# Kernel tuning notes

Measured on AMD Instinct MI355X. Metric: run time of the kernel, lower is better.

Reference implementation:

```python
import jax, jax.numpy as jnp
import numpy as np
from jax import lax

DN = ('NCHW', 'OIHW', 'NCHW')
NUM_CODES = 8192


def _conv(x, w, b):
    # Conv2d(k=4, s=2, p=1)
    y = lax.conv_general_dilated(x, w, (2, 2), ((1, 1), (1, 1)), dimension_numbers=DN)
    return y + b[None, :, None, None]


def _convT(x, w, b):
    # ConvTranspose2d(k=4, s=2, p=1) as lhs-dilated conv; kernel already in equivalent OIHW layout
    y = lax.conv_general_dilated(x, w, (1, 1), ((2, 2), (2, 2)), lhs_dilation=(2, 2), dimension_numbers=DN)
    return y + b[None, :, None, None]


def _aff(x, s, b):
    # eval-mode BatchNorm folded to per-channel affine
    return x * s[None, :, None, None] + b[None, :, None, None]


def _forward(x, ew1, eb1, bn1s, bn1b, ew2, eb2, bn2s, bn2b, ew3, eb3, bn3s, bn3b, ew4, eb4, embed, cluster_size, dw1, db1, dbn1s, dbn1b, dw2, db2, dbn2s, dbn2b, dw3, db3, dbn3s, dbn3b, dw4, db4):
    sg = lax.stop_gradient
    embed = sg(embed)          # codebook is a torch buffer -> no grad
    cluster_size = sg(cluster_size)
    relu = jax.nn.relu
    # ---- Encoder: 4 stride-2 convs ----
    h = relu(_aff(_conv(x, ew1, eb1), bn1s, bn1b))
    h = relu(_aff(_conv(h, ew2, eb2), bn2s, bn2b))
    h = relu(_aff(_conv(h, ew3, eb3), bn3s, bn3b))
    z = _conv(h, ew4, eb4)                       # [B, D, G, G]
    zt = jnp.transpose(z, (0, 2, 3, 1))          # [B, G, G, D]
    D = zt.shape[-1]
    flat = zt.reshape(-1, D)                     # [N, D]
    N = flat.shape[0]
    # ---- VQ: pairwise squared distance + argmin codebook lookup ----
    dist = (flat * flat).sum(1, keepdims=True) - 2.0 * (flat @ embed.T) + (embed * embed).sum(1)[None, :]
    soft = jax.nn.softmax(-dist, axis=-1)        # temperature = 1.0
    codes = jnp.argmin(dist, axis=1)             # [N]
    zq = embed[codes]                            # [N, D]
    commitment_loss = jnp.mean((flat - sg(zq)) ** 2)
    codebook_loss = jnp.mean((zq - sg(flat)) ** 2)
    avg_soft = soft.mean(0)
    usage_entropy = -(avg_soft * jnp.log(avg_soft + 1e-10)).sum()
    diversity_loss = -usage_entropy / float(np.log(NUM_CODES))
    zq_st = flat + sg(zq - flat)                 # straight-through estimator
    zq_grid = jnp.transpose(zq_st.reshape(zt.shape), (0, 3, 1, 2))  # [B, D, G, G]
    # ---- Decoder: 4 stride-2 transposed convs ----
    h = relu(_aff(_convT(zq_grid, dw1, db1), dbn1s, dbn1b))
    h = relu(_aff(_convT(h, dw2, db2), dbn2s, dbn2b))
    h = relu(_aff(_convT(h, dw3, db3), dbn3s, dbn3b))
    recon = jax.nn.sigmoid(_convT(h, dw4, db4))
    recon_loss = jnp.mean((recon - x) ** 2)
    # ---- usage stats (no-grad in torch) ----
    hard_avg = jnp.zeros(NUM_CODES, flat.dtype).at[codes].add(1.0) / N
    perplexity = jnp.exp(-(hard_avg * jnp.log(hard_avg + 1e-10)).sum())
    active_codes = (cluster_size > 1).sum()
    codes_grid = codes.reshape(zt.shape[:-1])
    return (recon, recon_loss, codes_grid, zq_grid, commitment_loss, codebook_loss, diversity_loss, usage_entropy, perplexity, active_codes)


def setup_inputs() -> dict:
    keys = iter(jax.random.split(jax.random.key(0), 64))
    def randn(shape, s=1.0):
        return jax.random.normal(next(keys), shape, jnp.float32) * s
    def randu(shape):
        return jax.random.uniform(next(keys), shape, dtype=jnp.float32)
    B, H = 32, 256
    return {
        'x': randu((B, 1, H, H)),
        'ew1': randn((64, 1, 4, 4), 0.25), 'eb1': randn((64,), 0.1),
        'bn1s': randu((64,)), 'bn1b': randn((64,), 0.1),
        'ew2': randn((64, 64, 4, 4), 0.03), 'eb2': randn((64,), 0.1),
        'bn2s': randu((64,)), 'bn2b': randn((64,), 0.1),
        'ew3': randn((128, 64, 4, 4), 0.03), 'eb3': randn((128,), 0.1),
        'bn3s': randu((128,)), 'bn3b': randn((128,), 0.1),
        'ew4': randn((64, 128, 4, 4), 0.02), 'eb4': randn((64,), 0.1),
        'embed': randn((8192, 64), 0.5),
        'cluster_size': jnp.ones((8192,), jnp.float32),
        'dw1': randn((128, 64, 4, 4), 0.03), 'db1': randn((128,), 0.1),
        'dbn1s': randu((128,)), 'dbn1b': randn((128,), 0.1),
        'dw2': randn((64, 128, 4, 4), 0.02), 'db2': randn((64,), 0.1),
        'dbn2s': randu((64,)), 'dbn2b': randn((64,), 0.1),
        'dw3': randn((64, 64, 4, 4), 0.03), 'db3': randn((64,), 0.1),
        'dbn3s': randu((64,)), 'dbn3b': randn((64,), 0.1),
        'dw4': randn((1, 64, 4, 4), 0.03), 'db4': randn((1,), 0.1),
    }


def reference(x, ew1, eb1, bn1s, bn1b, ew2, eb2, bn2s, bn2b, ew3, eb3, bn3s, bn3b, ew4, eb4, embed, cluster_size, dw1, db1, dbn1s, dbn1b, dw2, db2, dbn2s, dbn2b, dw3, db3, dbn3s, dbn3b, dw4, db4):
    return _forward(x, ew1, eb1, bn1s, bn1b, ew2, eb2, bn2s, bn2b, ew3, eb3, bn3s, bn3b, ew4, eb4, embed, cluster_size, dw1, db1, dbn1s, dbn1b, dw2, db2, dbn2s, dbn2b, dw3, db3, dbn3s, dbn3b, dw4, db4)
```

## Files before the change

kernel.cpp:

```cpp
#include <hip/hip_runtime.h>
#include <cstdint>
#include <cstddef>


#define DEVI __device__ __forceinline__

typedef short  short8 __attribute__((ext_vector_type(8)));
typedef __bf16 bf16x8 __attribute__((ext_vector_type(8)));
typedef float  f32x16 __attribute__((ext_vector_type(16)));

DEVI f32x16 MFMA(bf16x8 a, bf16x8 b, f32x16 c){
  return __builtin_amdgcn_mfma_f32_32x32x16_bf16(a, b, c, 0, 0, 0);
}

DEVI ushort f2bf(float f){
  unsigned u = __float_as_uint(f);
  unsigned r = (u + 0x7FFFu + ((u >> 16) & 1u)) >> 16;
  return (ushort)r;
}
DEVI float bf2f(ushort h){ return __uint_as_float(((unsigned)h) << 16); }

union U8 { short8 s; bf16x8 b; };
DEVI bf16x8 ldg8u(const ushort* p){
  U8 u; u.s = *(const short8*)p; return u.b;
}

DEVI float wred64(float v){
  #pragma unroll
  for (int off=32; off>0; off>>=1) v += __shfl_down(v, off, 64);
  return v;
}

#define O_RECON     0
#define O_RLOSS     2097152
#define O_CODES     2097153
#define O_ZQ        2105345
#define O_COMMIT    2629633
#define O_CB        2629634
#define O_DIV       2629635
#define O_UE        2629636
#define O_PERP      2629637
#define O_ACT       2629638

#define WS_R1       0ull
#define A3H_OFF     0ull
#define A3M_OFF     8912896ull
#define A3L_OFF     17825792ull
#define PP_OFF      33554432ull
#define MT_OFF      37748736ull
#define PARTA_OFF   41943040ull
#define A2H_OFF     134217728ull
#define A2M_OFF     151519232ull
#define A2L_OFF     168820736ull
#define EH_OFF      134217728ull
#define EM_OFF      135266304ull
#define EL_OFF      136314880ull
#define FH_OFF      137363456ull
#define FM_OFF      138412032ull
#define FL_OFF      139460608ull
#define D2H_OFF     134217728ull
#define D2L_OFF     151519232ull
#define D1H_OFF     168820736ull
#define D1L_OFF     177733632ull
#define WS_FLAT     186646528ull
#define WS_ZQP      188743680ull
#define WS_WT       191102976ull
#define WT_E2       (WS_WT)
#define WT_E3       (WT_E2 + 393216ull)
#define WT_E4       (WT_E3 + 786432ull)
#define WT_D1       (WT_E4 + 786432ull)
#define WT_D2       (WT_D1 + 524288ull)
#define WT_D3       (WT_D2 + 524288ull)
#define WS_W4       (WT_D3 + 262144ull)
#define WS_STATS    (WS_W4 + 4096ull)
#define ST_RMP      (WS_STATS)
#define ST_CNT      (ST_RMP + 65536ull)
#define ST_AVGS     (ST_CNT + 32768ull)
#define ST_ROWZI    (ST_AVGS + 32768ull)
#define ST_CODESQ   (ST_ROWZI + 32768ull)
#define ST_LOSS     (ST_CODESQ + 32768ull)
#define ST_ROWM     (ST_LOSS + 32768ull)

__global__ __launch_bounds__(256) void k_init(unsigned int* __restrict__ cnt,
                                              unsigned long long* __restrict__ rmp,
                                              float* __restrict__ loss)
{
  int i = blockIdx.x*256 + threadIdx.x;
  if (i < 8192){ cnt[i]=0u; rmp[i]=0xFFFFFFFFFFFFFFFFull; }
  if (i < 8) loss[i]=0.f;
}

__global__ __launch_bounds__(256) void k_wsplit(
    const float* __restrict__ src, ushort* __restrict__ dh,
    ushort* __restrict__ dm, ushort* __restrict__ dl,
    int OC, int CIN, int isT, int three)
{
  int i = blockIdx.x*256 + threadIdx.x;
  if (i >= 16*OC*CIN) return;
  int cin = i % CIN; int t = i / CIN; int oc = t % OC; int tap = t / OC;
  int st;
  if (isT){
    int pq = tap>>2, ab = tap&3;
    int p = pq>>1, q = pq&1, a = ab>>1, b = ab&1;
    st = (p + 2*a)*4 + (q + 2*b);
  } else st = tap;
  float v = src[((size_t)oc*CIN + cin)*16 + st];
  ushort h = f2bf(v); float r = v - bf2f(h);
  if (three){
    ushort m = f2bf(r); float r2 = r - bf2f(m);
    dm[i] = m; dl[i] = f2bf(r2);
  } else {
    dl[i] = f2bf(r);
  }
  dh[i] = h;
}

__global__ __launch_bounds__(256) void k_w4prep(const float* __restrict__ dw4,
                                                float* __restrict__ w4)
{
  int i = blockIdx.x*256 + threadIdx.x;
  if (i >= 1024) return;
  int c = i & 63; int t16 = i >> 6;
  int pq = t16 >> 2, ab = t16 & 3;
  int p = pq>>1, q = pq&1, a = ab>>1, b = ab&1;
  w4[i] = dw4[(size_t)c*16 + (p+2*a)*4 + (q+2*b)];
}

__global__ __launch_bounds__(256) void k_esplit(
    const float* __restrict__ src, ushort* __restrict__ dh,
    ushort* __restrict__ dm, ushort* __restrict__ dl)
{
  int i = blockIdx.x*256 + threadIdx.x;
  float v = src[i];
  ushort h = f2bf(v); float r1 = v - bf2f(h);
  ushort m = f2bf(r1); float r2 = r1 - bf2f(m);
  dh[i] = h; dm[i] = m; dl[i] = f2bf(r2);
}

__global__ __launch_bounds__(256) void k_zpad3(unsigned* __restrict__ b0,
                                               unsigned* __restrict__ b1,
                                               unsigned* __restrict__ b2,
                                               int rows, int Wp, int cwords)
{
  int i = blockIdx.x*256 + threadIdx.x;
  int total = rows*2*cwords;
  if (i >= total) return;
  int pos = i / cwords, cw = i % cwords;
  int row = pos >> 1, side = pos & 1;
  size_t w = ((size_t)row*Wp + (side ? (Wp-1) : 0))*cwords + cw;
  b0[w] = 0u;
  if (b1) b1[w] = 0u;
  if (b2) b2[w] = 0u;
}

__global__ __launch_bounds__(256) void enc_conv1(
    const float* __restrict__ x, const float* __restrict__ w,
    const float* __restrict__ cb_, const float* __restrict__ bns,
    const float* __restrict__ bnb, float* __restrict__ out)
{
  __shared__ __align__(16) float sIn[34][36];
  __shared__ __align__(16) float sW[64][16];
  int b = blockIdx.x;
  int t = b & 63, n = b >> 6;
  int ty = t >> 3, tx = t & 7;
  int oy0 = ty*16, ox0 = tx*16;
  int iy0 = 2*oy0 - 1, ix0 = 2*ox0 - 1;
  int tid = threadIdx.x;
  int spg = tid & 31, og = tid >> 5;
  int sy = spg >> 1, x0 = (spg & 1)*8;

  if (tid < 64){
    const float* wp = w + tid*16;
    *(float4*)&sW[tid][0]  = *(const float4*)(wp);
    *(float4*)&sW[tid][4]  = *(const float4*)(wp+4);
    *(float4*)&sW[tid][8]  = *(const float4*)(wp+8);
    *(float4*)&sW[tid][12] = *(const float4*)(wp+12);
  }
  for (int e = tid; e < 34*34; e += 256){
    int rr = e/34, cc = e%34;
    int iy = iy0+rr, ix = ix0+cc;
    float v = 0.f;
    if ((unsigned)iy < 256u && (unsigned)ix < 256u)
      v = x[(size_t)n*65536 + iy*256 + ix];
    sIn[rr][cc] = v;
  }
  __syncthreads();

  float acc[8][8];
  #pragma unroll
  for (int j=0;j<8;j++)
    #pragma unroll
    for (int xi=0;xi<8;xi++) acc[j][xi]=0.f;

  #pragma unroll
  for (int ky=0; ky<4; ky++){
    int riy = 2*sy + ky;
    float seg[20];
    #pragma unroll
    for (int i=0;i<5;i++){
      float4 v = *(const float4*)&sIn[riy][2*x0 + 4*i];
      seg[4*i+0]=v.x; seg[4*i+1]=v.y; seg[4*i+2]=v.z; seg[4*i+3]=v.w;
    }
    #pragma unroll
    for (int j=0;j<8;j++){
      float4 w4v = *(const float4*)&sW[og*8+j][ky*4];
      #pragma unroll
      for (int xi=0; xi<8; xi++){
        acc[j][xi] = fmaf(seg[2*xi+0], w4v.x,
                     fmaf(seg[2*xi+1], w4v.y,
                     fmaf(seg[2*xi+2], w4v.z,
                     fmaf(seg[2*xi+3], w4v.w, acc[j][xi]))));
      }
    }
  }

  float sc[8], sh[8];
  #pragma unroll
  for (int j=0;j<8;j++){
    int oc = og*8+j;
    sc[j] = bns[oc];
    sh[j] = fmaf(cb_[oc], sc[j], bnb[oc]);
  }
  int oy = oy0 + sy;
  #pragma unroll
  for (int xi=0; xi<8; xi++){
    int oxg = ox0 + x0 + xi;
    float* op = out + (((size_t)n*128 + oy)*128 + oxg)*64 + og*8;
    float4 q0, q1;
    q0.x = fmaxf(fmaf(acc[0][xi], sc[0], sh[0]), 0.f);
    q0.y = fmaxf(fmaf(acc[1][xi], sc[1], sh[1]), 0.f);
    q0.z = fmaxf(fmaf(acc[2][xi], sc[2], sh[2]), 0.f);
    q0.w = fmaxf(fmaf(acc[3][xi], sc[3], sh[3]), 0.f);
    q1.x = fmaxf(fmaf(acc[4][xi], sc[4], sh[4]), 0.f);
    q1.y = fmaxf(fmaf(acc[5][xi], sc[5], sh[5]), 0.f);
    q1.z = fmaxf(fmaf(acc[6][xi], sc[6], sh[6]), 0.f);
    q1.w = fmaxf(fmaf(acc[7][xi], sc[7], sh[7]), 0.f);
    *(float4*)op     = q0;
    *(float4*)(op+4) = q1;
  }
}

template<int CIN, int OC, int OUTW, int OUTH, int INW, int INH, bool XPAD,
         int INMODE, int OUTMODE>
__global__ __launch_bounds__(256) void enc_conv(
    const float* __restrict__ in,
    const ushort* __restrict__ aH, const ushort* __restrict__ aM,
    const ushort* __restrict__ aL,
    const ushort* __restrict__ wtH, const ushort* __restrict__ wtM,
    const ushort* __restrict__ wtL,
    const float* __restrict__ cb_, const float* __restrict__ bns,
    const float* __restrict__ bnb,
    float* __restrict__ outF,
    ushort* __restrict__ oH, ushort* __restrict__ oM, ushort* __restrict__ oL,
    int nOcg)
{
  constexpr int INWP  = (INMODE==1) ? (INW+2) : (XPAD ? (INW+2) : INW);
  constexpr int WP    = INW + 2;
  constexpr int NROWS = 64 / OUTW;
  constexpr int AELEM = NROWS * WP * CIN;
  constexpr int BCIN  = (CIN > 64) ? 64 : CIN;
  constexpr int BELEM = 64 * BCIN;
  constexpr int SCRSZ = (3*BELEM*2 > 64*68*4) ? 3*BELEM*2 : 64*68*4;

  __shared__ __align__(16) ushort sAh[AELEM], sAm[AELEM], sAl[AELEM];
  __shared__ __align__(16) char sScr[SCRSZ];
  ushort* sBh = (ushort*)sScr;
  ushort* sBm = sBh + BELEM;
  ushort* sBl = sBm + BELEM;
  float*  sC  = (float*)sScr;

  int b = blockIdx.x;
  int ocg = b % nOcg; b /= nOcg;
  int yb  = b % (OUTH/NROWS); b /= (OUTH/NROWS);
  int n = b;
  int oy0 = yb * NROWS, oc0 = ocg * 64;

  int tid = threadIdx.x;
  int l = tid & 63, wave = tid >> 6;
  int wm = wave >> 1, wn = wave & 1;
  int r = l & 31, kp = l >> 5;
  int idx = wm*32 + r;
  int oy_off = idx / OUTW, ox = idx % OUTW;

  f32x16 acc;
  #pragma unroll
  for (int i=0;i<16;i++) acc[i] = 0.f;

  const size_t nbase = (size_t)n * INH * INWP * CIN;

  for (int ky = 0; ky < 4; ky++){
    __syncthreads();
    for (int c = tid; c < AELEM/8; c += 256){
      int j  = c / (WP*CIN/8);
      int rm = c % (WP*CIN/8);
      int lx = rm / (CIN/8);
      int c8 = (rm % (CIN/8)) * 8;
      int iy = 2*(oy0 + j) - 1 + ky;
      bool ok = (unsigned)iy < (unsigned)INH;
      unsigned off = (unsigned)(((j*WP + lx)*CIN + c8)*2) ^ ((((unsigned)lx>>1)&7u)<<4);
      if constexpr (INMODE == 0){
        int gx = XPAD ? lx : (lx - 1);
        if (!XPAD) ok = ok && ((unsigned)gx < (unsigned)INW);
        float4 v0 = {0,0,0,0}, v1 = {0,0,0,0};
        if (ok){
          const float* s = in + nbase + ((size_t)iy*INWP + gx)*CIN + c8;
          v0 = *(const float4*)s; v1 = *(const float4*)(s+4);
        }
        float vv[8] = {v0.x,v0.y,v0.z,v0.w,v1.x,v1.y,v1.z,v1.w};
        short8 hh, mm, ll;
        #pragma unroll
        for (int e=0;e<8;e++){
          ushort h = f2bf(vv[e]); float r1 = vv[e] - bf2f(h);
          ushort m = f2bf(r1);    float r2 = r1 - bf2f(m);
          hh[e] = (short)h; mm[e] = (short)m; ll[e] = (short)f2bf(r2);
        }
        *(short8*)((char*)sAh + off) = hh;
        *(short8*)((char*)sAm + off) = mm;
        *(short8*)((char*)sAl + off) = ll;
      } else {
        short8 vh = {0,0,0,0,0,0,0,0}, vm = vh, vl = vh;
        if (ok){
          size_t s = nbase + ((size_t)iy*INWP + lx)*CIN + c8;
          vh = *(const short8*)(aH + s);
          vm = *(const short8*)(aM + s);
          vl = *(const short8*)(aL + s);
        }
        *(short8*)((char*)sAh + off) = vh;
        *(short8*)((char*)sAm + off) = vm;
        *(short8*)((char*)sAl + off) = vl;
      }
    }
    for (int kx = 0; kx < 4; kx++){
      int tap = ky*4 + kx;
      for (int ch = 0; ch < CIN; ch += BCIN){
        __syncthreads();
        for (int c = tid; c < BELEM/8; c += 256){
          int oc = c / (BCIN/8);
          int c8 = (c % (BCIN/8)) * 8;
          size_t s = ((size_t)tap*OC + oc0 + oc)*CIN + ch + c8;
          unsigned off = (unsigned)((oc*BCIN + c8)*2) ^ (((unsigned)oc&7u)<<4);
          *(short8*)((char*)sBh + off) = *(const short8*)(wtH + s);
          *(short8*)((char*)sBm + off) = *(const short8*)(wtM + s);
          *(short8*)((char*)sBl + off) = *(const short8*)(wtL + s);
        }
        __syncthreads();
        int lx = 2*ox + kx;
        unsigned asw  = ((((unsigned)lx>>1)&7u)<<4);
        unsigned alin = (unsigned)(((oy_off*WP + lx)*CIN)*2);
        int ocl = wn*32 + r;
        unsigned bsw  = (((unsigned)ocl&7u)<<4);
        unsigned blin = (unsigned)((ocl*BCIN)*2);
        #pragma unroll
        for (int ct = 0; ct < BCIN/16; ct++){
          unsigned kbA = (unsigned)((ch + ct*16 + kp*8)*2);
          unsigned kbB = (unsigned)((ct*16 + kp*8)*2);
          unsigned ao = (alin + kbA) ^ asw;
          unsigned bo = (blin + kbB) ^ bsw;
          bf16x8 ah = *(const bf16x8*)((char*)sAh + ao);
          bf16x8 am = *(const bf16x8*)((char*)sAm + ao);
          bf16x8 al = *(const bf16x8*)((char*)sAl + ao);
          bf16x8 bh = *(const bf16x8*)((char*)sBh + bo);
          bf16x8 bm = *(const bf16x8*)((char*)sBm + bo);
          bf16x8 bl = *(const bf16x8*)((char*)sBl + bo);
          acc = MFMA(ah, bh, acc);
          acc = MFMA(ah, bm, acc);
          acc = MFMA(am, bh, acc);
          acc = MFMA(ah, bl, acc);
          acc = MFMA(am, bm, acc);
          acc = MFMA(al, bh, acc);
        }
      }
    }
  }
  __syncthreads();
  #pragma unroll
  for (int q = 0; q < 16; q++){
    int rowt = (q&3) + 8*(q>>2) + 4*kp;
    sC[(wm*32 + rowt)*68 + wn*32 + r] = acc[q];
  }
  __syncthreads();
  {
    int m = tid >> 2, qq = tid & 3;
    int oc = oc0 + qq*16;
    int oyg = oy0 + m / OUTW;
    int oxg = m % OUTW;
    if constexpr (OUTMODE == 1){
      size_t row = (size_t)n*256 + oyg*16 + oxg;
      float* op = outF + row*64 + qq*16;
      size_t pb = row*64 + qq*16;
      short8 hv[2], mv[2], lv[2];
      #pragma unroll
      for (int i=0;i<16;i++){
        float v = sC[m*68 + qq*16 + i] + cb_[oc+i];
        op[i] = v;
        ushort h = f2bf(v); float r1 = v - bf2f(h);
        ushort mm = f2bf(r1); float r2 = r1 - bf2f(mm);
        hv[i>>3][i&7]=(short)h; mv[i>>3][i&7]=(short)mm; lv[i>>3][i&7]=(short)f2bf(r2);
      }
      *(short8*)(oH + pb) = hv[0]; *(short8*)(oH + pb + 8) = hv[1];
      *(short8*)(oM + pb) = mv[0]; *(short8*)(oM + pb + 8) = mv[1];
      *(short8*)(oL + pb) = lv[0]; *(short8*)(oL + pb + 8) = lv[1];
    } else {
      size_t pbase = (((size_t)n*OUTH + oyg)*(OUTW+2) + oxg + 1)*OC + oc;
      short8 hv[2], mv[2], lv[2];
      #pragma unroll
      for (int i=0;i<16;i++){
        float s1 = bns[oc+i];
        float s2 = fmaf(cb_[oc+i], s1, bnb[oc+i]);
        float v = fmaxf(fmaf(sC[m*68 + qq*16 + i], s1, s2), 0.f);
        ushort h = f2bf(v); float r1 = v - bf2f(h);
        ushort mm = f2bf(r1); float r2 = r1 - bf2f(mm);
        hv[i>>3][i&7]=(short)h; mv[i>>3][i&7]=(short)mm; lv[i>>3][i&7]=(short)f2bf(r2);
      }
      *(short8*)(oH + pbase)   = hv[0]; *(short8*)(oH + pbase+8) = hv[1];
      *(short8*)(oM + pbase)   = mv[0]; *(short8*)(oM + pbase+8) = mv[1];
      *(short8*)(oL + pbase)   = lv[0]; *(short8*)(oL + pbase+8) = lv[1];
    }
  }
}

__global__ __launch_bounds__(256) void k_codesq(const float* __restrict__ embed,
                                                float* __restrict__ codesq)
{
  int j = blockIdx.x*4 + (threadIdx.x>>6);
  int c = threadIdx.x & 63;
  float e = embed[(size_t)j*64 + c];
  float s = wred64(e*e);
  if (c==0) codesq[j] = s;
}

DEVI float rmp_minval(unsigned long long v){
  unsigned skey = (unsigned)(v >> 32);
  unsigned u = (skey & 0x80000000u) ? (skey ^ 0x80000000u) : ~skey;
  return __uint_as_float(u);
}

__global__ __launch_bounds__(256) void vq_min(
    const ushort* __restrict__ fH, const ushort* __restrict__ fM,
    const ushort* __restrict__ fL,
    const ushort* __restrict__ eH, const ushort* __restrict__ eM,
    const ushort* __restrict__ eL,
    const float* __restrict__ codesq,
    unsigned long long* __restrict__ rmp,
    float* __restrict__ Pp, float* __restrict__ Mt)
{
  __shared__ __align__(16) ushort sAh[128*64], sAm[128*64], sAl[128*64];
  int cblk = blockIdx.x & 63, fblk = blockIdx.x >> 6;
  int code0 = cblk*128, f0 = fblk*128;
  int tid = threadIdx.x, l = tid&63, wave = tid>>6;
  int wm = wave>>1, wn = wave&1, r = l&31, kp = l>>5;

  for (int c = tid; c < 1024; c += 256){
    int rr = c >> 3, c8 = (c & 7)*8;
    size_t s = (size_t)(code0+rr)*64 + c8;
    unsigned off = (unsigned)((rr*64 + c8)*2) ^ (((unsigned)rr&7u)<<4);
    *(short8*)((char*)sAh + off) = *(const short8*)(eH + s);
    *(short8*)((char*)sAm + off) = *(const short8*)(eM + s);
    *(short8*)((char*)sAl + off) = *(const short8*)(eL + s);
  }
  __syncthreads();

  f32x16 acc[2][2];
  #pragma unroll
  for (int mt=0;mt<2;mt++)
    #pragma unroll
    for (int nt=0;nt<2;nt++)
      #pragma unroll
      for (int i=0;i<16;i++) acc[mt][nt][i]=0.f;

  #pragma unroll
  for (int ks=0; ks<4; ks++){
    unsigned kb = (unsigned)((ks*16 + kp*8)*2);
    int ko = ks*16 + kp*8;
    bf16x8 Ah[2],Am[2],Al[2],Bh[2],Bm[2],Bl[2];
    #pragma unroll
    for (int mt=0;mt<2;mt++){
      int rowi = wm*64 + mt*32 + r;
      unsigned o = ((unsigned)(rowi*128) + kb) ^ (((unsigned)rowi&7u)<<4);
      Ah[mt] = *(const bf16x8*)((char*)sAh + o);
      Am[mt] = *(const bf16x8*)((char*)sAm + o);
      Al[mt] = *(const bf16x8*)((char*)sAl + o);
    }
    #pragma unroll
    for (int nt=0;nt<2;nt++){
      int coli = f0 + wn*64 + nt*32 + r;
      size_t bo = (size_t)coli*64 + ko;
      Bh[nt] = ldg8u(fH + bo);
      Bm[nt] = ldg8u(fM + bo);
      Bl[nt] = ldg8u(fL + bo);
    }
    #pragma unroll
    for (int mt=0;mt<2;mt++)
      #pragma unroll
      for (int nt=0;nt<2;nt++){
        acc[mt][nt] = MFMA(Ah[mt], Bh[nt], acc[mt][nt]);
        acc[mt][nt] = MFMA(Ah[mt], Bm[nt], acc[mt][nt]);
        acc[mt][nt] = MFMA(Am[mt], Bh[nt], acc[mt][nt]);
        acc[mt][nt] = MFMA(Ah[mt], Bl[nt], acc[mt][nt]);
        acc[mt][nt] = MFMA(Am[mt], Bm[nt], acc[mt][nt]);
        acc[mt][nt] = MFMA(Al[mt], Bh[nt], acc[mt][nt]);
      }
  }

  float cqv[2][16];
  #pragma unroll
  for (int mt=0; mt<2; mt++)
    #pragma unroll
    for (int g=0; g<4; g++){
      float4 cv = *(const float4*)(codesq + code0 + wm*64 + mt*32 + 8*g + 4*kp);
      cqv[mt][4*g+0]=cv.x; cqv[mt][4*g+1]=cv.y;
      cqv[mt][4*g+2]=cv.z; cqv[mt][4*g+3]=cv.w;
    }

  #pragma unroll
  for (int nt=0; nt<2; nt++){
    int col = f0 + wn*64 + nt*32 + r;
    unsigned long long kmin = 0xFFFFFFFFFFFFFFFFull;
    #pragma unroll
    for (int mt=0; mt<2; mt++)
      #pragma unroll
      for (int q=0; q<16; q++){
        float d = cqv[mt][q] - 2.f*acc[mt][nt][q];
        int code = code0 + wm*64 + mt*32 + (q&3) + 8*(q>>2) + 4*kp;
        unsigned u = __float_as_uint(d);
        unsigned sgn = (unsigned)((int)u >> 31);
        unsigned skey = u ^ (sgn | 0x80000000u);
        unsigned long long key = (((unsigned long long)skey)<<32) | (unsigned)code;
        if (key < kmin) kmin = key;
      }
    unsigned long long o2 = __shfl_xor(kmin, 32, 64);
    if (o2 < kmin) kmin = o2;
// ... 77 lines not shown
    #pragma unroll
    for (int mt=0;mt<2;mt++){
      int rowi = wm*64 + mt*32 + r;
      unsigned o = ((unsigned)(rowi*128) + kb) ^ (((unsigned)rowi&7u)<<4);
      Ah[mt] = *(const bf16x8*)((char*)sAh + o);
      Am[mt] = *(const bf16x8*)((char*)sAm + o);
      Al[mt] = *(const bf16x8*)((char*)sAl + o);
    }
    #pragma unroll
    for (int nt=0;nt<2;nt++){
      int coli = c0 + wn*64 + nt*32 + r;
      size_t bo = (size_t)coli*64 + ko;
      Bh[nt] = ldg8u(eH + bo);
      Bm[nt] = ldg8u(eM + bo);
      Bl[nt] = ldg8u(eL + bo);
    }
    #pragma unroll
    for (int mt=0;mt<2;mt++)
      #pragma unroll
      for (int nt=0;nt<2;nt++){
        acc[mt][nt] = MFMA(Ah[mt], Bh[nt], acc[mt][nt]);
        acc[mt][nt] = MFMA(Ah[mt], Bm[nt], acc[mt][nt]);
        acc[mt][nt] = MFMA(Am[mt], Bh[nt], acc[mt][nt]);
        acc[mt][nt] = MFMA(Ah[mt], Bl[nt], acc[mt][nt]);
        acc[mt][nt] = MFMA(Am[mt], Bm[nt], acc[mt][nt]);
        acc[mt][nt] = MFMA(Al[mt], Bh[nt], acc[mt][nt]);
      }
  }

  float cq[2];
  cq[0] = codesq[c0 + wn*64 + r];
  cq[1] = codesq[c0 + wn*64 + 32 + r];
  float colacc[2] = {0.f, 0.f};
  #pragma unroll
  for (int mt=0; mt<2; mt++){
    #pragma unroll
    for (int q=0; q<16; q++){
      int rowt = (q&3) + 8*(q>>2) + 4*kp;
      int grow = row0 + wm*64 + mt*32 + rowt;
      float mi = rowm[grow];
      float zi = rowzi[grow];
      #pragma unroll
      for (int nt=0; nt<2; nt++){
        float d = cq[nt] - 2.f*acc[mt][nt][q];
        colacc[nt] = fmaf(__expf(mi - d), zi, colacc[nt]);
      }
    }
  }
  #pragma unroll
  for (int nt=0; nt<2; nt++){
    float o = __shfl_xor(colacc[nt], 32, 64);
    colacc[nt] += o;
    if (l < 32) atomicAdd(&colbuf[wn*64 + nt*32 + r], colacc[nt]);
  }
  __syncthreads();
  if (tid < 128)
    partA[(size_t)rb*8192 + c0 + tid] = colbuf[tid];
}

__global__ __launch_bounds__(256) void k_avgred(const float* __restrict__ partA,
                                                float* __restrict__ avgs)
{
  int j = blockIdx.x*256 + threadIdx.x;
  float s = 0.f;
  for (int rb = 0; rb < 64; rb++)
    s += partA[(size_t)rb*8192 + j];
  avgs[j] = s;
}

__global__ __launch_bounds__(256) void vq_post(
    const float* __restrict__ flat, const float* __restrict__ embed,
    const unsigned long long* __restrict__ rmp,
    float* __restrict__ out_codes, float* __restrict__ out_zq,
    ushort* __restrict__ zqPh, ushort* __restrict__ zqPl,
    float* __restrict__ loss, unsigned int* __restrict__ cnt)
{
  int r = blockIdx.x*4 + (threadIdx.x>>6);
  int c = threadIdx.x & 63;
  unsigned j = (unsigned)(rmp[r] & 0xFFFFFFFFull);
  float e = embed[(size_t)j*64 + c];
  float f = flat[(size_t)r*64 + c];
  int n = r>>8, rem = r&255, gy = rem>>4, gx = rem&15;
  out_zq[(((size_t)n*64 + c)*16 + gy)*16 + gx] = e;
  ushort h = f2bf(e);
  size_t pz = (((size_t)n*16 + gy)*18 + gx + 1)*64 + c;
  zqPh[pz] = h; zqPl[pz] = f2bf(e - bf2f(h));
  float d = f - e;
  float s2 = wred64(d*d);
  if (c==0){
    out_codes[r] = (float)j;
    atomicAdd(cnt + j, 1u);
    atomicAdd(loss + 1, s2);
  }
}

template<int CIN, int OC, int SW, int SH, bool OUTPAD, int OMODE, int NPAR>
__global__ __launch_bounds__(256) void dec_convT_m(
    const ushort* __restrict__ inH, const ushort* __restrict__ inL,
    const ushort* __restrict__ wtH, const ushort* __restrict__ wtL,
    const float* __restrict__ db, const float* __restrict__ bns,
    const float* __restrict__ bnb,
    ushort* __restrict__ oH, ushort* __restrict__ oL, int nOcg)
{
  constexpr int TR    = 64 / SW;
  constexpr int NRA   = TR + ((NPAR==4) ? 2 : 1);
  constexpr int WPin  = SW + 2;
  constexpr int AELEM = NRA * WPin * CIN;
  constexpr int OUTH  = 2*SH;
  constexpr int OW    = OUTPAD ? (2*SW+2) : (2*SW);

  __shared__ __align__(16) ushort sAh[AELEM], sAl[AELEM];
  __shared__ __align__(16) float sC[64*68];

  int b = blockIdx.x;
  int p_blk = 0;
  if (NPAR == 2){ p_blk = b & 1; b >>= 1; }
  int ocg = b % nOcg; b /= nOcg;
  int tb = b % (SH/TR); b /= (SH/TR);
  int n = b;
  int t0 = tb * TR, oc0 = ocg * 64;
  const int ROWBASE = (NPAR==4) ? -1 : (p_blk - 1);

  int tid = threadIdx.x, l = tid&63, wave = tid>>6;
  int wm = wave>>1, wn = wave&1;
  int r = l&31, kp = l>>5;
  int idx = wm*32 + r;
  int t_off = idx / SW, s = idx % SW;
  int ocl = oc0 + wn*32 + r;

  for (int c = tid; c < AELEM/8; c += 256){
    int j  = c / (WPin*CIN/8);
    int rm = c % (WPin*CIN/8);
    int lx = rm / (CIN/8);
    int c8 = (rm % (CIN/8)) * 8;
    int giy = t0 + ROWBASE + j;
    bool ok = (unsigned)giy < (unsigned)SH;
    short8 vh = {0,0,0,0,0,0,0,0}, vl = {0,0,0,0,0,0,0,0};
    if (ok){
      size_t sidx = (((size_t)n*SH + giy)*WPin + lx)*CIN + c8;
      vh = *(const short8*)(inH + sidx);
      vl = *(const short8*)(inL + sidx);
    }
    unsigned off = (unsigned)(((j*WPin + lx)*CIN + c8)*2) ^ (((unsigned)lx&7u)<<4);
    *(short8*)((char*)sAh + off) = vh;
    *(short8*)((char*)sAl + off) = vl;
  }
  __syncthreads();

  for (int pr = 0; pr < NPAR; pr++){
    int p2 = (NPAR==4) ? (pr>>1) : p_blk;
    int q2 = (NPAR==4) ? (pr&1)  : pr;
    int par = p2*2 + q2;

    f32x16 acc;
    #pragma unroll
    for (int i=0;i<16;i++) acc[i]=0.f;

    for (int ab = 0; ab < 4; ab++){
      int a = ab>>1, bb = ab&1;
      int rs = t_off + ((NPAR==4) ? (p2 + a) : a);
      int lx = s + q2 + bb;
      unsigned asw  = (((unsigned)lx&7u)<<4);
      unsigned alin = (unsigned)(((rs*WPin + lx)*CIN)*2);
      size_t brow = ((size_t)(par*4 + ab)*OC + ocl)*CIN;
      #pragma unroll
      for (int ct = 0; ct < CIN/16; ct++){
        int ko = ct*16 + kp*8;
        unsigned ao = (alin + (unsigned)(ko*2)) ^ asw;
        bf16x8 ah = *(const bf16x8*)((char*)sAh + ao);
        bf16x8 al = *(const bf16x8*)((char*)sAl + ao);
        bf16x8 bh = ldg8u(wtH + brow + ko);
        bf16x8 bl = ldg8u(wtL + brow + ko);
        acc = MFMA(ah, bh, acc);
        acc = MFMA(ah, bl, acc);
        acc = MFMA(al, bh, acc);
      }
    }

    __syncthreads();
    #pragma unroll
    for (int qre = 0; qre < 16; qre++){
      int rowt = (qre&3) + 8*(qre>>2) + 4*kp;
      sC[(wm*32 + rowt)*68 + wn*32 + r] = acc[qre];
    }
    __syncthreads();
    {
      int m = tid >> 2, qq = tid & 3;
      int oc = oc0 + qq*16;
      int y  = 2*(t0 + m/SW) + p2;
      int xs = m % SW;
      int xp = OUTPAD ? (2*xs + q2 + 1) : (2*xs + q2);
      size_t base = (((size_t)n*OUTH + y)*OW + xp)*OC + oc;
      if constexpr (OMODE == 2){
        short8 h0[2];
        #pragma unroll
        for (int i=0;i<16;i++){
          float s1 = bns[oc+i];
          float s2 = fmaf(db[oc+i], s1, bnb[oc+i]);
          float v = fmaxf(fmaf(sC[m*68 + qq*16 + i], s1, s2), 0.f);
          h0[i>>3][i&7] = (short)f2bf(v);
        }
        *(short8*)(oH + base)     = h0[0];
        *(short8*)(oH + base + 8) = h0[1];
      } else {
        short8 h0[2], l0[2];
        #pragma unroll
        for (int i=0;i<16;i++){
          float s1 = bns[oc+i];
          float s2 = fmaf(db[oc+i], s1, bnb[oc+i]);
          float v = fmaxf(fmaf(sC[m*68 + qq*16 + i], s1, s2), 0.f);
          ushort h = f2bf(v);
          ushort lo = f2bf(v - bf2f(h));
          h0[i>>3][i&7]=(short)h; l0[i>>3][i&7]=(short)lo;
        }
        *(short8*)(oH + base)     = h0[0];
        *(short8*)(oH + base + 8) = h0[1];
        *(short8*)(oL + base)     = l0[0];
        *(short8*)(oL + base + 8) = l0[1];
      }
    }
  }
}

__global__ __launch_bounds__(256) void dec_convT4(
    const ushort* __restrict__ d3, const float* __restrict__ w4,
    const float* __restrict__ db4, const float* __restrict__ xref,
    float* __restrict__ recon, float* __restrict__ loss)
{
  __shared__ __align__(16) float sT[10*10*68];
  __shared__ __align__(16) float sWt[16*64];
  __shared__ float red[4];
  int b = blockIdx.x;
  int t = b & 255, n = b >> 8;
  int ty = t >> 4, tx = t & 15;
  int y0 = ty*16, x0 = tx*16;
  int r0 = y0/2 - 1, c0 = x0/2 - 1;
  int tid = threadIdx.x;

  *(float4*)&sWt[tid*4] = *(const float4*)(w4 + tid*4);

  const ushort* base = d3 + (size_t)n*128*128*64;
  for (int e = tid; e < 800; e += 256){
    int rr = e/80; int rem = e%80; int cc = rem/8; int c8 = (rem%8)*8;
    int gr = r0+rr, gc = c0+cc;
    short8 v = {0,0,0,0,0,0,0,0};
    if ((unsigned)gr<128u && (unsigned)gc<128u)
      v = *(const short8*)(base + ((size_t)gr*128+gc)*64 + c8);
    float* dst = &sT[(rr*10+cc)*68 + c8];
    float4 f0, f1;
    f0.x = bf2f((ushort)v[0]); f0.y = bf2f((ushort)v[1]);
    f0.z = bf2f((ushort)v[2]); f0.w = bf2f((ushort)v[3]);
    f1.x = bf2f((ushort)v[4]); f1.y = bf2f((ushort)v[5]);
    f1.z = bf2f((ushort)v[6]); f1.w = bf2f((ushort)v[7]);
    *(float4*)dst     = f0;
    *(float4*)(dst+4) = f1;
  }
  __syncthreads();

  int sy = tid>>4, sx = tid&15;
  int p = sy&1, q = sx&1;
  int lr0 = (sy>>1)+p, lc0 = (sx>>1)+q;
  int par = p*2+q;
  float4 a4 = {0,0,0,0};
  #pragma unroll
  for (int a=0;a<2;a++){
    #pragma unroll
    for (int bb=0;bb<2;bb++){
      const float* ip = &sT[((lr0+a)*10 + lc0+bb)*68];
      const float* wp = &sWt[(par*4+a*2+bb)*64];
      #pragma unroll
      for (int c=0;c<64;c+=4){
        float4 v  = *(const float4*)(ip+c);
        float4 wv = *(const float4*)(wp+c);
        a4.x = fmaf(v.x, wv.x, a4.x);
        a4.y = fmaf(v.y, wv.y, a4.y);
        a4.z = fmaf(v.z, wv.z, a4.z);
        a4.w = fmaf(v.w, wv.w, a4.w);
      }
    }
  }
  float acc = (a4.x + a4.y) + (a4.z + a4.w);
  float v = acc + db4[0];
  float rcn = 1.f/(1.f + __expf(-v));
  int y = y0+sy, x = x0+sx;
  size_t oi = (size_t)n*65536 + (size_t)y*256 + x;
  recon[oi] = rcn;
  float d = rcn - xref[oi];
  float s2 = wred64(d*d);
  if ((tid & 63)==0) red[tid>>6] = s2;
  __syncthreads();
  if (tid==0) atomicAdd(loss + 0, red[0]+red[1]+red[2]+red[3]);
}

__global__ __launch_bounds__(256) void k_final(
    const float* __restrict__ avgs, const unsigned int* __restrict__ cnt,
    const float* __restrict__ cluster, const float* __restrict__ loss,
    float* __restrict__ dout)
{
  __shared__ float red[3][4];
  int tid = threadIdx.x;
  float e1=0.f, e2=0.f, ac=0.f;
  for (int j=tid; j<8192; j+=256){
    float a = avgs[j] * (1.f/8192.f);
    e1 += a * __logf(a + 1e-10f);
    float h = (float)cnt[j] * (1.f/8192.f);
    e2 += h * __logf(h + 1e-10f);
    ac += (cluster[j] > 1.f) ? 1.f : 0.f;
  }
  e1 = wred64(e1); e2 = wred64(e2); ac = wred64(ac);
  int wv = tid >> 6;
  if ((tid & 63)==0){ red[0][wv]=e1; red[1][wv]=e2; red[2][wv]=ac; }
  __syncthreads();
  if (tid==0){
    float s1 = red[0][0]+red[0][1]+red[0][2]+red[0][3];
    float s2 = red[1][0]+red[1][1]+red[1][2]+red[1][3];
    float s3 = red[2][0]+red[2][1]+red[2][2]+red[2][3];
    float ue = -s1;
    dout[O_RLOSS]  = loss[0] * (1.f/2097152.f);
    float cc = loss[1] * (1.f/524288.f);
    dout[O_COMMIT] = cc;
    dout[O_CB]     = cc;
    dout[O_DIV]    = -ue / 9.010913347279288f;
    dout[O_UE]     = ue;
    dout[O_PERP]   = __expf(-s2);
    dout[O_ACT]    = s3;
  }
}

extern "C" void kernel_launch(void* const* d_in, const int* in_sizes, int n_in,
                              void* d_out, int out_size, void* d_ws, size_t ws_size,
                              hipStream_t stream)
{
  (void)in_sizes; (void)n_in; (void)out_size; (void)ws_size;
  const float* x     = (const float*)d_in[0];
  const float* ew1   = (const float*)d_in[1];
  const float* eb1   = (const float*)d_in[2];
  const float* bn1s  = (const float*)d_in[3];
  const float* bn1b  = (const float*)d_in[4];
  const float* ew2   = (const float*)d_in[5];
  const float* eb2   = (const float*)d_in[6];
  const float* bn2s  = (const float*)d_in[7];
  const float* bn2b  = (const float*)d_in[8];
  const float* ew3   = (const float*)d_in[9];
  const float* eb3   = (const float*)d_in[10];
  const float* bn3s  = (const float*)d_in[11];
  const float* bn3b  = (const float*)d_in[12];
  const float* ew4   = (const float*)d_in[13];
  const float* eb4   = (const float*)d_in[14];
  const float* embed = (const float*)d_in[15];
  const float* clsz  = (const float*)d_in[16];
  const float* dw1   = (const float*)d_in[17];
  const float* db1   = (const float*)d_in[18];
  const float* dbn1s = (const float*)d_in[19];
  const float* dbn1b = (const float*)d_in[20];
  const float* dw2   = (const float*)d_in[21];
  const float* db2   = (const float*)d_in[22];
  const float* dbn2s = (const float*)d_in[23];
  const float* dbn2b = (const float*)d_in[24];
  const float* dw3   = (const float*)d_in[25];
  const float* db3   = (const float*)d_in[26];
  const float* dbn3s = (const float*)d_in[27];
  const float* dbn3b = (const float*)d_in[28];
  const float* dw4   = (const float*)d_in[29];
  const float* db4   = (const float*)d_in[30];

  float* out = (float*)d_out;
  uint8_t* wsb = (uint8_t*)d_ws;

  float*  A1   = (float*)(wsb + WS_R1);
  ushort* D3b  = (ushort*)(wsb + WS_R1);
  ushort* A3h  = (ushort*)(wsb + A3H_OFF);
  ushort* A3m  = (ushort*)(wsb + A3M_OFF);
  ushort* A3l  = (ushort*)(wsb + A3L_OFF);
  float*  Pp   = (float*)(wsb + PP_OFF);
  float*  Mt   = (float*)(wsb + MT_OFF);
  float*  partA= (float*)(wsb + PARTA_OFF);
  ushort* A2h  = (ushort*)(wsb + A2H_OFF);
  ushort* A2m  = (ushort*)(wsb + A2M_OFF);
  ushort* A2l  = (ushort*)(wsb + A2L_OFF);
  ushort* eH   = (ushort*)(wsb + EH_OFF);
  ushort* eM   = (ushort*)(wsb + EM_OFF);
  ushort* eL   = (ushort*)(wsb + EL_OFF);
  ushort* fH   = (ushort*)(wsb + FH_OFF);
  ushort* fM   = (ushort*)(wsb + FM_OFF);
  ushort* fL   = (ushort*)(wsb + FL_OFF);
  ushort* D1h  = (ushort*)(wsb + D1H_OFF);
  ushort* D1l  = (ushort*)(wsb + D1L_OFF);
  ushort* D2h  = (ushort*)(wsb + D2H_OFF);
  ushort* D2l  = (ushort*)(wsb + D2L_OFF);
  float*  flat = (float*)(wsb + WS_FLAT);
  ushort* zqPh = (ushort*)(wsb + WS_ZQP);
  ushort* zqPl = (ushort*)(wsb + WS_ZQP + 1179648ull);

  ushort* wE2h = (ushort*)(wsb + WT_E2);
  ushort* wE2m = wE2h + 65536;  ushort* wE2l = wE2m + 65536;
  ushort* wE3h = (ushort*)(wsb + WT_E3);
  ushort* wE3m = wE3h + 131072; ushort* wE3l = wE3m + 131072;
  ushort* wE4h = (ushort*)(wsb + WT_E4);
  ushort* wE4m = wE4h + 131072; ushort* wE4l = wE4m + 131072;
  ushort* wD1h = (ushort*)(wsb + WT_D1);
  ushort* wD1l = wD1h + 131072;
  ushort* wD2h = (ushort*)(wsb + WT_D2);
  ushort* wD2l = wD2h + 131072;
  ushort* wD3h = (ushort*)(wsb + WT_D3);
  ushort* wD3l = wD3h + 65536;
  float*  w4   = (float*)(wsb + WS_W4);

  unsigned long long* rmp = (unsigned long long*)(wsb + ST_RMP);
  unsigned int* cnt = (unsigned int*)(wsb + ST_CNT);
  float* avgs   = (float*)(wsb + ST_AVGS);
  float* rowzi  = (float*)(wsb + ST_ROWZI);
  float* codesq = (float*)(wsb + ST_CODESQ);
  float* loss   = (float*)(wsb + ST_LOSS);
  float* rowm   = (float*)(wsb + ST_ROWM);

  dim3 B(256);

  k_init<<<32, B, 0, stream>>>(cnt, rmp, loss);

  k_wsplit<<<256, B, 0, stream>>>(ew2, wE2h, wE2m, wE2l, 64, 64, 0, 1);
  k_wsplit<<<512, B, 0, stream>>>(ew3, wE3h, wE3m, wE3l, 128, 64, 0, 1);
  k_wsplit<<<512, B, 0, stream>>>(ew4, wE4h, wE4m, wE4l, 64, 128, 0, 1);
  k_wsplit<<<512, B, 0, stream>>>(dw1, wD1h, nullptr, wD1l, 128, 64, 1, 0);
  k_wsplit<<<512, B, 0, stream>>>(dw2, wD2h, nullptr, wD2l, 64, 128, 1, 0);
  k_wsplit<<<256, B, 0, stream>>>(dw3, wD3h, nullptr, wD3l, 64, 64, 1, 0);
  k_w4prep<<<4, B, 0, stream>>>(dw4, w4);

  k_zpad3<<<512, B, 0, stream>>>((unsigned*)A2h, (unsigned*)A2m, (unsigned*)A2l,
                                 32*64, 66, 32);
  k_zpad3<<<128, B, 0, stream>>>((unsigned*)zqPh, (unsigned*)zqPl, nullptr,
                                 32*16, 18, 32);

  enc_conv1<<<2048, B, 0, stream>>>(x, ew1, eb1, bn1s, bn1b, A1);
  enc_conv<64,64,64,64,128,128,false,0,0><<<2048, B, 0, stream>>>(
      A1, nullptr, nullptr, nullptr, wE2h, wE2m, wE2l, eb2, bn2s, bn2b,
      nullptr, A2h, A2m, A2l, 1);
  k_zpad3<<<512, B, 0, stream>>>((unsigned*)A3h, (unsigned*)A3m, (unsigned*)A3l,
                                 32*32, 34, 64);
  enc_conv<64,128,32,32,64,64,true,1,0><<<1024, B, 0, stream>>>(
      nullptr, A2h, A2m, A2l, wE3h, wE3m, wE3l, eb3, bn3s, bn3b,
      nullptr, A3h, A3m, A3l, 2);
  k_esplit<<<2048, B, 0, stream>>>(embed, eH, eM, eL);
  enc_conv<128,64,16,16,32,32,true,1,1><<<128, B, 0, stream>>>(
      nullptr, A3h, A3m, A3l, wE4h, wE4m, wE4l, eb4, eb4, eb4,
      flat, fH, fM, fL, 1);

  k_codesq<<<2048, B, 0, stream>>>(embed, codesq);

  vq_min<<<4096, B, 0, stream>>>(fH, fM, fL, eH, eM, eL, codesq, rmp, Pp, Mt);
  k_rowz2<<<32, B, 0, stream>>>(rmp, Pp, Mt, rowzi, rowm);
  vq_avg<<<4096, B, 0, stream>>>(fH, fM, fL, eH, eM, eL, codesq, rowm, rowzi, partA);
  k_avgred<<<32, B, 0, stream>>>(partA, avgs);

  vq_post<<<2048, B, 0, stream>>>(flat, embed, rmp, out + O_CODES, out + O_ZQ,
                                  zqPh, zqPl, loss, cnt);

  k_zpad3<<<512, B, 0, stream>>>((unsigned*)D1h, (unsigned*)D1l, nullptr, 32*32, 34, 64);
  k_zpad3<<<512, B, 0, stream>>>((unsigned*)D2h, (unsigned*)D2l, nullptr, 32*64, 66, 32);

  dec_convT_m<64,128,16,16,true,0,4><<<256, B, 0, stream>>>(
      zqPh, zqPl, wD1h, wD1l, db1, dbn1s, dbn1b, D1h, D1l, 2);
  dec_convT_m<128,64,32,32,true,0,2><<<1024, B, 0, stream>>>(
      D1h, D1l, wD2h, wD2l, db2, dbn2s, dbn2b, D2h, D2l, 1);
  dec_convT_m<64,64,64,64,false,2,4><<<2048, B, 0, stream>>>(
      D2h, D2l, wD3h, wD3l, db3, dbn3s, dbn3b, D3b, nullptr, 1);
  dec_convT4<<<8192, B, 0, stream>>>(D3b, w4, db4, x, out + O_RECON, loss);

  k_final<<<1, B, 0, stream>>>(avgs, cnt, clsz, loss, out);
}
```

Measured before the change: 1.000 ms.

## Merge prep kernels, register-prefetch conv weights, split MFMA accumulators

Merges the init, weight-split, w4 prep and zero-pad launches into one multi-role prep kernel, and merges the two decoder pad kernels into one, so fewer small launches are issued. In enc_conv, the next stage's weight tile is prefetched into registers while the current stage computes. Both enc_conv and dec_convT_m now alternate MFMAs between two accumulators, which shortens the dependency chain. The prefetch raises register pressure and the extra accumulator costs more VGPRs, which may lower occupancy.

```diff
diff --git a/kernel.cpp b/kernel.cpp
--- a/kernel.cpp
+++ b/kernel.cpp
@@ -24,6 +24,7 @@
 DEVI bf16x8 ldg8u(const ushort* p){
   U8 u; u.s = *(const short8*)p; return u.b;
 }
+DEVI bf16x8 s2b(short8 s){ U8 u; u.s = s; return u.b; }
 
 DEVI float wred64(float v){
   #pragma unroll
@@ -81,21 +82,9 @@
 #define ST_LOSS     (ST_CODESQ + 32768ull)
 #define ST_ROWM     (ST_LOSS + 32768ull)
 
-__global__ __launch_bounds__(256) void k_init(unsigned int* __restrict__ cnt,
-                                              unsigned long long* __restrict__ rmp,
-                                              float* __restrict__ loss)
-{
-  int i = blockIdx.x*256 + threadIdx.x;
-  if (i < 8192){ cnt[i]=0u; rmp[i]=0xFFFFFFFFFFFFFFFFull; }
-  if (i < 8) loss[i]=0.f;
-}
-
-__global__ __launch_bounds__(256) void k_wsplit(
-    const float* __restrict__ src, ushort* __restrict__ dh,
-    ushort* __restrict__ dm, ushort* __restrict__ dl,
-    int OC, int CIN, int isT, int three)
-{
-  int i = blockIdx.x*256 + threadIdx.x;
+DEVI void wsplit_body(int i, const float* src, ushort* dh, ushort* dm,
+                      ushort* dl, int OC, int CIN, int isT, int three)
+{
   if (i >= 16*OC*CIN) return;
   int cin = i % CIN; int t = i / CIN; int oc = t % OC; int tap = t / OC;
   int st;
@@ -115,34 +104,9 @@
   dh[i] = h;
 }
 
-__global__ __launch_bounds__(256) void k_w4prep(const float* __restrict__ dw4,
-                                                float* __restrict__ w4)
-{
-  int i = blockIdx.x*256 + threadIdx.x;
-  if (i >= 1024) return;
-  int c = i & 63; int t16 = i >> 6;
-  int pq = t16 >> 2, ab = t16 & 3;
-  int p = pq>>1, q = pq&1, a = ab>>1, b = ab&1;
-  w4[i] = dw4[(size_t)c*16 + (p+2*a)*4 + (q+2*b)];
-}
-
-__global__ __launch_bounds__(256) void k_esplit(
-    const float* __restrict__ src, ushort* __restrict__ dh,
-    ushort* __restrict__ dm, ushort* __restrict__ dl)
-{
-  int i = blockIdx.x*256 + threadIdx.x;
-  float v = src[i];
-  ushort h = f2bf(v); float r1 = v - bf2f(h);
-  ushort m = f2bf(r1); float r2 = r1 - bf2f(m);
-  dh[i] = h; dm[i] = m; dl[i] = f2bf(r2);
-}
-
-__global__ __launch_bounds__(256) void k_zpad3(unsigned* __restrict__ b0,
-                                               unsigned* __restrict__ b1,
-                                               unsigned* __restrict__ b2,
-                                               int rows, int Wp, int cwords)
-{
-  int i = blockIdx.x*256 + threadIdx.x;
+DEVI void zpad_body(int i, unsigned* b0, unsigned* b1, unsigned* b2,
+                    int rows, int Wp, int cwords)
+{
   int total = rows*2*cwords;
   if (i >= total) return;
   int pos = i / cwords, cw = i % cwords;
@@ -151,6 +115,76 @@
   b0[w] = 0u;
   if (b1) b1[w] = 0u;
   if (b2) b2[w] = 0u;
+}
+
+__global__ __launch_bounds__(256) void k_prep(
+    const float* __restrict__ ew2, const float* __restrict__ ew3,
+    const float* __restrict__ ew4, const float* __restrict__ dw1,
+    const float* __restrict__ dw2, const float* __restrict__ dw3,
+    const float* __restrict__ dw4,
+    ushort* wE2h, ushort* wE2m, ushort* wE2l,
+    ushort* wE3h, ushort* wE3m, ushort* wE3l,
+    ushort* wE4h, ushort* wE4m, ushort* wE4l,
+    ushort* wD1h, ushort* wD1l, ushort* wD2h, ushort* wD2l,
+    ushort* wD3h, ushort* wD3l, float* w4,
+    unsigned* A2h, unsigned* A2m, unsigned* A2l,
+    unsigned* zqPh, unsigned* zqPl,
+    unsigned int* cnt, unsigned long long* rmp, float* loss)
+{
+  int b = blockIdx.x, tid = threadIdx.x;
+  if (b < 32){
+    int i = b*256 + tid;
+    if (i < 8192){ cnt[i]=0u; rmp[i]=0xFFFFFFFFFFFFFFFFull; }
+    if (i < 8) loss[i]=0.f;
+  } else if (b < 288){
+    wsplit_body((b-32)*256 + tid, ew2, wE2h, wE2m, wE2l, 64, 64, 0, 1);
+  } else if (b < 800){
+    wsplit_body((b-288)*256 + tid, ew3, wE3h, wE3m, wE3l, 128, 64, 0, 1);
+  } else if (b < 1312){
+    wsplit_body((b-800)*256 + tid, ew4, wE4h, wE4m, wE4l, 64, 128, 0, 1);
+  } else if (b < 1824){
+    wsplit_body((b-1312)*256 + tid, dw1, wD1h, nullptr, wD1l, 128, 64, 1, 0);
+  } else if (b < 2336){
+    wsplit_body((b-1824)*256 + tid, dw2, wD2h, nullptr, wD2l, 64, 128, 1, 0);
+  } else if (b < 2592){
+    wsplit_body((b-2336)*256 + tid, dw3, wD3h, nullptr, wD3l, 64, 64, 1, 0);
+  } else if (b < 2596){
+    int i = (b-2592)*256 + tid;
+    if (i < 1024){
+      int c = i & 63; int t16 = i >> 6;
+      int pq = t16 >> 2, ab = t16 & 3;
+      int p = pq>>1, q = pq&1, a = ab>>1, bb = ab&1;
+      w4[i] = dw4[(size_t)c*16 + (p+2*a)*4 + (q+2*bb)];
+    }
+  } else if (b < 3108){
+    zpad_body((b-2596)*256 + tid, A2h, A2m, A2l, 32*64, 66, 32);
+  } else {
+    zpad_body((b-3108)*256 + tid, zqPh, zqPl, nullptr, 32*16, 18, 32);
+  }
+}
+
+__global__ __launch_bounds__(256) void k_zpadA3(unsigned* b0, unsigned* b1,
+                                                unsigned* b2)
+{
+  zpad_body(blockIdx.x*256 + threadIdx.x, b0, b1, b2, 32*32, 34, 64);
+}
+__global__ __launch_bounds__(256) void k_zpadD(unsigned* d1h, unsigned* d1l,
+                                               unsigned* d2h, unsigned* d2l)
+{
+  int b = blockIdx.x;
+  if (b < 512) zpad_body(b*256 + threadIdx.x, d1h, d1l, nullptr, 32*32, 34, 64);
+  else zpad_body((b-512)*256 + threadIdx.x, d2h, d2l, nullptr, 32*64, 66, 32);
+}
+
+__global__ __launch_bounds__(256) void k_esplit(
+    const float* __restrict__ src, ushort* __restrict__ dh,
+    ushort* __restrict__ dm, ushort* __restrict__ dl)
+{
+  int i = blockIdx.x*256 + threadIdx.x;
+  float v = src[i];
+  ushort h = f2bf(v); float r1 = v - bf2f(h);
+  ushort m = f2bf(r1); float r2 = r1 - bf2f(m);
+  dh[i] = h; dm[i] = m; dl[i] = f2bf(r2);
 }
 
 __global__ __launch_bounds__(256) void enc_conv1(
@@ -260,6 +294,9 @@
   constexpr int AELEM = NROWS * WP * CIN;
   constexpr int BCIN  = (CIN > 64) ? 64 : CIN;
   constexpr int BELEM = 64 * BCIN;
+  constexpr int NCH   = CIN / BCIN;
+  constexpr int NSTG  = 16 * NCH;
+  constexpr int PFI   = BELEM / 8 / 256;
   constexpr int SCRSZ = (3*BELEM*2 > 64*68*4) ? 3*BELEM*2 : 64*68*4;
 
   __shared__ __align__(16) ushort sAh[AELEM], sAm[AELEM], sAl[AELEM];
@@ -282,11 +319,30 @@
   int idx = wm*32 + r;
   int oy_off = idx / OUTW, ox = idx % OUTW;
 
-  f32x16 acc;
-  #pragma unroll
-  for (int i=0;i<16;i++) acc[i] = 0.f;
+  int pfoc[PFI], pfc8[PFI];
+  #pragma unroll
+  for (int it=0; it<PFI; it++){
+    int c = tid + it*256;
+    pfoc[it] = c / (BCIN/8);
+    pfc8[it] = (c % (BCIN/8)) * 8;
+  }
+  short8 pf0[PFI], pf1[PFI], pf2[PFI];
+  {
+    #pragma unroll
+    for (int it=0; it<PFI; it++){
+      size_t off = ((size_t)oc0 + pfoc[it])*CIN + pfc8[it];
+      pf0[it] = *(const short8*)(wtH + off);
+      pf1[it] = *(const short8*)(wtM + off);
+      pf2[it] = *(const short8*)(wtL + off);
+    }
+  }
+
+  f32x16 acc0, acc1;
+  #pragma unroll
+  for (int i=0;i<16;i++){ acc0[i]=0.f; acc1[i]=0.f; }
 
   const size_t nbase = (size_t)n * INH * INWP * CIN;
+  int sidx = 0;
 
   for (int ky = 0; ky < 4; ky++){
     __syncthreads();
@@ -331,19 +387,31 @@
       }
     }
     for (int kx = 0; kx < 4; kx++){
-      int tap = ky*4 + kx;
-      for (int ch = 0; ch < CIN; ch += BCIN){
+      for (int chi = 0; chi < NCH; chi++){
+        int ch = chi * BCIN;
         __syncthreads();
-        for (int c = tid; c < BELEM/8; c += 256){
-          int oc = c / (BCIN/8);
-          int c8 = (c % (BCIN/8)) * 8;
-          size_t s = ((size_t)tap*OC + oc0 + oc)*CIN + ch + c8;
-          unsigned off = (unsigned)((oc*BCIN + c8)*2) ^ (((unsigned)oc&7u)<<4);
-          *(short8*)((char*)sBh + off) = *(const short8*)(wtH + s);
-          *(short8*)((char*)sBm + off) = *(const short8*)(wtM + s);
-          *(short8*)((char*)sBl + off) = *(const short8*)(wtL + s);
+        #pragma unroll
+        for (int it=0; it<PFI; it++){
+          unsigned off = (unsigned)((pfoc[it]*BCIN + pfc8[it])*2)
+                         ^ (((unsigned)pfoc[it]&7u)<<4);
+          *(short8*)((char*)sBh + off) = pf0[it];
+          *(short8*)((char*)sBm + off) = pf1[it];
+          *(short8*)((char*)sBl + off) = pf2[it];
         }
         __syncthreads();
+        if (sidx + 1 < NSTG){
+          int ns = sidx + 1;
+          int ntap = ns / NCH, nchi = ns % NCH;
+          #pragma unroll
+          for (int it=0; it<PFI; it++){
+            size_t off = ((size_t)ntap*OC + oc0 + pfoc[it])*CIN
+                         + nchi*BCIN + pfc8[it];
+            pf0[it] = *(const short8*)(wtH + off);
+            pf1[it] = *(const short8*)(wtM + off);
+            pf2[it] = *(const short8*)(wtL + off);
+          }
+        }
+        sidx++;
         int lx = 2*ox + kx;
         unsigned asw  = ((((unsigned)lx>>1)&7u)<<4);
         unsigned alin = (unsigned)(((oy_off*WP + lx)*CIN)*2);
@@ -362,12 +430,12 @@
           bf16x8 bh = *(const bf16x8*)((char*)sBh + bo);
           bf16x8 bm = *(const bf16x8*)((char*)sBm + bo);
           bf16x8 bl = *(const bf16x8*)((char*)sBl + bo);
-          acc = MFMA(ah, bh, acc);
-          acc = MFMA(ah, bm, acc);
-          acc = MFMA(am, bh, acc);
-          acc = MFMA(ah, bl, acc);
-          acc = MFMA(am, bm, acc);
-          acc = MFMA(al, bh, acc);
+          acc0 = MFMA(ah, bh, acc0);
+          acc1 = MFMA(ah, bm, acc1);
+          acc0 = MFMA(am, bh, acc0);
+          acc1 = MFMA(ah, bl, acc1);
+          acc0 = MFMA(am, bm, acc0);
+          acc1 = MFMA(al, bh, acc1);
         }
       }
     }
@@ -376,7 +444,7 @@
   #pragma unroll
   for (int q = 0; q < 16; q++){
     int rowt = (q&3) + 8*(q>>2) + 4*kp;
-    sC[(wm*32 + rowt)*68 + wn*32 + r] = acc[q];
+    sC[(wm*32 + rowt)*68 + wn*32 + r] = acc0[q] + acc1[q];
   }
   __syncthreads();
   {
@@ -760,9 +828,9 @@
     int q2 = (NPAR==4) ? (pr&1)  : pr;
     int par = p2*2 + q2;
 
-    f32x16 acc;
-    #pragma unroll
-    for (int i=0;i<16;i++) acc[i]=0.f;
+    f32x16 acc0, acc1;
+    #pragma unroll
+    for (int i=0;i<16;i++){ acc0[i]=0.f; acc1[i]=0.f; }
 
     for (int ab = 0; ab < 4; ab++){
       int a = ab>>1, bb = ab&1;
@@ -779,9 +847,9 @@
         bf16x8 al = *(const bf16x8*)((char*)sAl + ao);
         bf16x8 bh = ldg8u(wtH + brow + ko);
         bf16x8 bl = ldg8u(wtL + brow + ko);
-        acc = MFMA(ah, bh, acc);
-        acc = MFMA(ah, bl, acc);
-        acc = MFMA(al, bh, acc);
+        acc0 = MFMA(ah, bh, acc0);
+        acc1 = MFMA(ah, bl, acc1);
+        acc0 = MFMA(al, bh, acc0);
       }
     }
 
@@ -789,7 +857,7 @@
     #pragma unroll
     for (int qre = 0; qre < 16; qre++){
       int rowt = (qre&3) + 8*(qre>>2) + 4*kp;
-      sC[(wm*32 + rowt)*68 + wn*32 + r] = acc[qre];
+      sC[(wm*32 + rowt)*68 + wn*32 + r] = acc0[qre] + acc1[qre];
     }
     __syncthreads();
     {
@@ -1024,27 +1092,19 @@
 
   dim3 B(256);
 
-  k_init<<<32, B, 0, stream>>>(cnt, rmp, loss);
-
-  k_wsplit<<<256, B, 0, stream>>>(ew2, wE2h, wE2m, wE2l, 64, 64, 0, 1);
-  k_wsplit<<<512, B, 0, stream>>>(ew3, wE3h, wE3m, wE3l, 128, 64, 0, 1);
-  k_wsplit<<<512, B, 0, stream>>>(ew4, wE4h, wE4m, wE4l, 64, 128, 0, 1);
-  k_wsplit<<<512, B, 0, stream>>>(dw1, wD1h, nullptr, wD1l, 128, 64, 1, 0);
-  k_wsplit<<<512, B, 0, stream>>>(dw2, wD2h, nullptr, wD2l, 64, 128, 1, 0);
-  k_wsplit<<<256, B, 0, stream>>>(dw3, wD3h, nullptr, wD3l, 64, 64, 1, 0);
-  k_w4prep<<<4, B, 0, stream>>>(dw4, w4);
-
-  k_zpad3<<<512, B, 0, stream>>>((unsigned*)A2h, (unsigned*)A2m, (unsigned*)A2l,
-                                 32*64, 66, 32);
-  k_zpad3<<<128, B, 0, stream>>>((unsigned*)zqPh, (unsigned*)zqPl, nullptr,
-                                 32*16, 18, 32);
+  k_prep<<<3236, B, 0, stream>>>(
+      ew2, ew3, ew4, dw1, dw2, dw3, dw4,
+      wE2h, wE2m, wE2l, wE3h, wE3m, wE3l, wE4h, wE4m, wE4l,
+      wD1h, wD1l, wD2h, wD2l, wD3h, wD3l, w4,
+      (unsigned*)A2h, (unsigned*)A2m, (unsigned*)A2l,
+      (unsigned*)zqPh, (unsigned*)zqPl,
+      cnt, rmp, loss);
 
   enc_conv1<<<2048, B, 0, stream>>>(x, ew1, eb1, bn1s, bn1b, A1);
   enc_conv<64,64,64,64,128,128,false,0,0><<<2048, B, 0, stream>>>(
       A1, nullptr, nullptr, nullptr, wE2h, wE2m, wE2l, eb2, bn2s, bn2b,
       nullptr, A2h, A2m, A2l, 1);
-  k_zpad3<<<512, B, 0, stream>>>((unsigned*)A3h, (unsigned*)A3m, (unsigned*)A3l,
-                                 32*32, 34, 64);
+  k_zpadA3<<<512, B, 0, stream>>>((unsigned*)A3h, (unsigned*)A3m, (unsigned*)A3l);
   enc_conv<64,128,32,32,64,64,true,1,0><<<1024, B, 0, stream>>>(
       nullptr, A2h, A2m, A2l, wE3h, wE3m, wE3l, eb3, bn3s, bn3b,
       nullptr, A3h, A3m, A3l, 2);
@@ -1063,8 +1123,8 @@
   vq_post<<<2048, B, 0, stream>>>(flat, embed, rmp, out + O_CODES, out + O_ZQ,
                                   zqPh, zqPl, loss, cnt);
 
-  k_zpad3<<<512, B, 0, stream>>>((unsigned*)D1h, (unsigned*)D1l, nullptr, 32*32, 34, 64);
-  k_zpad3<<<512, B, 0, stream>>>((unsigned*)D2h, (unsigned*)D2l, nullptr, 32*64, 66, 32);
+  k_zpadD<<<1024, B, 0, stream>>>((unsigned*)D1h, (unsigned*)D1l,
+                                  (unsigned*)D2h, (unsigned*)D2l);
 
   dec_convT_m<64,128,16,16,true,0,4><<<256, B, 0, stream>>>(
       zqPh, zqPl, wD1h, wD1l, db1, dbn1s, dbn1b, D1h, D1l, 2);
```

After: 944.4 us. 5.6% less time.
